# Performance work log

Hardware: AMD Instinct MI355X
Metric: run time of the kernel (lower is better)

Reference implementation:

```python
import jax, jax.numpy as jnp
import numpy as np

B, NUM_HIDDENS, H, W = 32, 128, 64, 64
EMB_DIM = 64
NUM_EMB = 512
COMMITMENT_COST = 0.25


def setup_inputs() -> dict:
    key = jax.random.key(0)
    ks = jax.random.split(key, 5)
    return {
        "bottom_encoding": jax.random.normal(ks[0], (B, NUM_HIDDENS, H, W), jnp.float32),
        "pre_w": jax.random.normal(ks[1], (EMB_DIM, NUM_HIDDENS), jnp.float32) / np.sqrt(NUM_HIDDENS).astype(np.float32),
        "pre_b": jnp.zeros((EMB_DIM,), jnp.float32),
        "codebook": jax.random.uniform(ks[2], (NUM_EMB, EMB_DIM), jnp.float32, -1.0 / NUM_EMB, 1.0 / NUM_EMB),
        "post_w": jax.random.normal(ks[3], (NUM_HIDDENS, EMB_DIM), jnp.float32) / np.sqrt(EMB_DIM).astype(np.float32),
        "post_b": jnp.zeros((NUM_HIDDENS,), jnp.float32),
    }


def reference(bottom_encoding, pre_w, pre_b, codebook, post_w, post_b):
    # pre-VQ 1x1 conv: [B, num_hiddens, H, W] -> [B, emb_dim, H, W]
    x = jnp.einsum('bchw,oc->bohw', bottom_encoding, pre_w) + pre_b[None, :, None, None]
    # BCHW -> BHWC, flatten to [N, D]
    z = jnp.transpose(x, (0, 2, 3, 1))
    flat = z.reshape(-1, EMB_DIM)
    # squared euclidean distances to codebook: [N, K]
    dists = (jnp.sum(flat * flat, axis=1, keepdims=True)
             + jnp.sum(codebook * codebook, axis=1)[None, :]
             - 2.0 * flat @ codebook.T)
    idx = jnp.argmin(dists, axis=1)              # [N] int
    quantized = codebook[idx].reshape(z.shape)   # gather, [B, H, W, D]
    # VQ losses
    e_latent_loss = jnp.mean((jax.lax.stop_gradient(quantized) - z) ** 2)
    q_latent_loss = jnp.mean((quantized - jax.lax.stop_gradient(z)) ** 2)
    loss = q_latent_loss + COMMITMENT_COST * e_latent_loss
    # straight-through estimator
    quantized_st = z + jax.lax.stop_gradient(quantized - z)
    # perplexity of codebook usage
    counts = jnp.zeros((NUM_EMB,), jnp.float32).at[idx].add(1.0)
    avg_probs = counts / idx.shape[0]
    perplexity = jnp.exp(-jnp.sum(avg_probs * jnp.log(avg_probs + 1e-10)))
    # post-VQ 1x1 conv: [B, emb_dim, H, W] -> [B, num_hiddens, H, W]
    qc = jnp.transpose(quantized_st, (0, 3, 1, 2))
    global_decode = jnp.einsum('bchw,oc->bohw', qc, post_w) + post_b[None, :, None, None]
    indices = idx.reshape(B, H, W)
    return loss, global_decode, perplexity, indices
```

## Files before the change

### kernel.cpp

```cpp
#include <hip/hip_runtime.h>

typedef unsigned short u16;
typedef unsigned int u32;
typedef __attribute__((ext_vector_type(8))) short short8v;
typedef __attribute__((ext_vector_type(4))) float f32x4;

#define NPX   131072
#define CHN   128
#define HWN   4096
#define EMB   64
#define NCODE 512

#define WS_HIST 0
#define WS_LOSS 2048
#define WS_CC   4096
#define WS_PWT  8192
#define WS_IDX  40960
#define WS_DT   303104


#define MFMA(a, b, c) __builtin_amdgcn_mfma_f32_16x16x32_bf16((a), (b), (c), 0, 0, 0)

#define SPLIT3(V, HH, MM, LL) {                          \
  u32 zb_ = __float_as_uint(V);                          \
  HH = zb_ >> 16;                                        \
  float fh_ = __uint_as_float(HH << 16);                 \
  float r1_ = __fsub_rn((V), fh_);                       \
  MM = __float_as_uint(r1_) >> 16;                       \
  float fm_ = __uint_as_float(MM << 16);                 \
  float r2_ = __fsub_rn(r1_, fm_);                       \
  LL = __float_as_uint(r2_) >> 16; }

__device__ __forceinline__ float rec3(u32 hb, u32 mb, u32 lb) {
  return __fadd_rn(__fadd_rn(__uint_as_float(hb), __uint_as_float(mb)),
                   __uint_as_float(lb));
}

__global__ __launch_bounds__(256) void vq_init(const float* __restrict__ preW,
                                               const float* __restrict__ cb,
                                               const float* __restrict__ postW,
                                               const float* __restrict__ postB,
                                               float* __restrict__ preWT,
                                               float* __restrict__ cc,
                                               u16* __restrict__ ch,
                                               u16* __restrict__ cm,
                                               u16* __restrict__ cl,
                                               float* __restrict__ DT,
                                               u32* __restrict__ wz) {
  int bid = blockIdx.x, tid = threadIdx.x;
  int idx = bid * 256 + tid;
  {
    int k = idx >> 7, o = idx & 127;
    const float* q = cb + k * EMB;
    const float* w = postW + o * EMB;
    float a0 = 0.f, a1 = 0.f, a2 = 0.f, a3 = 0.f;
#pragma unroll
    for (int dd = 0; dd < 64; dd += 4) {
      a0 = fmaf(q[dd + 0], w[dd + 0], a0);
      a1 = fmaf(q[dd + 1], w[dd + 1], a1);
      a2 = fmaf(q[dd + 2], w[dd + 2], a2);
      a3 = fmaf(q[dd + 3], w[dd + 3], a3);
    }
    DT[(size_t)k * 128 + o] = ((a0 + a1) + (a2 + a3)) + postB[o];
  }
  if (bid == 0) {
    for (int i = tid; i < CHN * EMB; i += 256) {
      int c = i >> 6, d = i & 63;
      preWT[i] = preW[d * CHN + c];
    }
  } else if (bid == 1) {
    for (int t = tid; t < NCODE; t += 256) {
      const float* row = cb + t * EMB;
      float r[8];
#pragma unroll
      for (int j = 0; j < 8; ++j) r[j] = __fmul_rn(row[j], row[j]);
#pragma unroll
      for (int b = 1; b < 8; ++b)
#pragma unroll
        for (int j = 0; j < 8; ++j)
          r[j] = __fadd_rn(r[j], __fmul_rn(row[b * 8 + j], row[b * 8 + j]));
      cc[t] = __fadd_rn(__fadd_rn(__fadd_rn(r[0], r[1]), __fadd_rn(r[2], r[3])),
                        __fadd_rn(__fadd_rn(r[4], r[5]), __fadd_rn(r[6], r[7])));
      int tile = t >> 4, rr = t & 15;
      for (int d = 0; d < EMB; ++d) {
        float v = row[d];
        u32 hh, mm, ll;
        SPLIT3(v, hh, mm, ll)
        size_t ti = (size_t)tile * 1024 + (size_t)(d >> 3) * 128 + rr * 8 + (d & 7);
        ch[ti] = (u16)hh;
        cm[ti] = (u16)mm;
        cl[ti] = (u16)ll;
      }
    }
  } else if (bid == 2) {
    for (int i = tid; i < 513; i += 256) wz[i] = 0;
  }
}

__global__ __launch_bounds__(256) void vq_pre(const float* __restrict__ A,
                                              const float* __restrict__ preWT,
                                              const float* __restrict__ preB,
                                              u16* __restrict__ zh,
                                              u16* __restrict__ zm,
                                              u16* __restrict__ zl) {
  int bid = blockIdx.x;
  int ph = bid & 511, dh = bid >> 9;
  int d0 = dh << 4;
  int p = ph * 256 + threadIdx.x;
  int b = p >> 12, hw = p & 4095;
  const float* Ab = A + (size_t)b * CHN * HWN + hw;

  float z[16];
#pragma unroll
  for (int d = 0; d < 16; ++d) z[d] = 0.f;
  for (int c = 0; c < CHN; c += 4) {
    float a0 = Ab[(size_t)(c + 0) * HWN];
    float a1 = Ab[(size_t)(c + 1) * HWN];
    float a2 = Ab[(size_t)(c + 2) * HWN];
    float a3 = Ab[(size_t)(c + 3) * HWN];
    const float* w = preWT + c * EMB + d0;
#pragma unroll
    for (int d = 0; d < 16; ++d) z[d] = __fadd_rn(z[d], __fmul_rn(a0, w[d]));
    w += EMB;
#pragma unroll
    for (int d = 0; d < 16; ++d) z[d] = __fadd_rn(z[d], __fmul_rn(a1, w[d]));
    w += EMB;
#pragma unroll
    for (int d = 0; d < 16; ++d) z[d] = __fadd_rn(z[d], __fmul_rn(a2, w[d]));
    w += EMB;
#pragma unroll
    for (int d = 0; d < 16; ++d) z[d] = __fadd_rn(z[d], __fmul_rn(a3, w[d]));
  }
#pragma unroll
  for (int d = 0; d < 16; ++d) z[d] = __fadd_rn(z[d], preB[d0 + d]);

  u32 hwd[8], mwd[8], lwd[8];
#pragma unroll
  for (int i = 0; i < 16; ++i) {
    u32 hh, mm, ll;
    SPLIT3(z[i], hh, mm, ll)
    int wdi = i >> 1;
    if ((i & 1) == 0) { hwd[wdi] = hh; mwd[wdi] = mm; lwd[wdi] = ll; }
    else { hwd[wdi] |= hh << 16; mwd[wdi] |= mm << 16; lwd[wdi] |= ll << 16; }
  }
  int tile = p >> 4, rr = p & 15;
  size_t base = (size_t)tile * 1024 + (size_t)(dh * 2) * 128 + rr * 8;
#pragma unroll
  for (int q = 0; q < 2; ++q) {
    size_t off = base + (size_t)q * 128;
    *(uint4*)(zh + off) = make_uint4(hwd[4*q], hwd[4*q+1], hwd[4*q+2], hwd[4*q+3]);
    *(uint4*)(zm + off) = make_uint4(mwd[4*q], mwd[4*q+1], mwd[4*q+2], mwd[4*q+3]);
    *(uint4*)(zl + off) = make_uint4(lwd[4*q], lwd[4*q+1], lwd[4*q+2], lwd[4*q+3]);
  }
}


#define LOADB(T) { size_t ob_ = (size_t)(T) * 1024 + l8;                         \
  Bh0 = *(const short8v*)(ch + ob_); Bh1 = *(const short8v*)(ch + ob_ + 512);    \
  Bm0 = *(const short8v*)(cm + ob_); Bm1 = *(const short8v*)(cm + ob_ + 512);    \
  Bl0 = *(const short8v*)(cl + ob_); Bl1 = *(const short8v*)(cl + ob_ + 512); }

#define COMP(T) {                                                       \
  float ccv_ = scc[((T) << 4) + mcol];                                  \
  _Pragma("unroll")                                                     \
  for (int mt = 0; mt < 2; ++mt) {                                      \
    f32x4 acc = {0.f, 0.f, 0.f, 0.f};                                   \
    acc = MFMA(Ah[mt][0], Bh0, acc); acc = MFMA(Ah[mt][1], Bh1, acc);   \
    acc = MFMA(Am[mt][0], Bh0, acc); acc = MFMA(Am[mt][1], Bh1, acc);   \
    acc = MFMA(Ah[mt][0], Bm0, acc); acc = MFMA(Ah[mt][1], Bm1, acc);   \
    acc = MFMA(Am[mt][0], Bm0, acc); acc = MFMA(Am[mt][1], Bm1, acc);   \
    acc = MFMA(Al[mt][0], Bh0, acc); acc = MFMA(Al[mt][1], Bh1, acc);   \
    acc = MFMA(Ah[mt][0], Bl0, acc); acc = MFMA(Ah[mt][1], Bl1, acc);   \
    acc = MFMA(Al[mt][0], Bm0, acc); acc = MFMA(Al[mt][1], Bm1, acc);   \
    acc = MFMA(Am[mt][0], Bl0, acc); acc = MFMA(Am[mt][1], Bl1, acc);   \
    _Pragma("unroll")                                                   \
    for (int r = 0; r < 4; ++r) {                                       \
      float dist_ = __fadd_rn(__fadd_rn(zzr[mt][r], ccv_), -2.0f * acc[r]); \
      if (dist_ < best[mt][r]) { best[mt][r] = dist_; bidx[mt][r] = ((T) << 4) + mcol; } \
    } } }

__global__ __launch_bounds__(256, 4) void vq_search(const u16* __restrict__ zh,
                                                    const u16* __restrict__ zm,
                                                    const u16* __restrict__ zl,
                                                    const u16* __restrict__ ch,
                                                    const u16* __restrict__ cm,
                                                    const u16* __restrict__ cl,
                                                    const float* __restrict__ cc,
                                                    const float* __restrict__ cb,
                                                    u16* __restrict__ wsIdx,
                                                    float* __restrict__ outIdx,
                                                    float* __restrict__ lossAcc,
                                                    unsigned int* __restrict__ hist) {
  __shared__ float scc[512];
  __shared__ float zs[4][2][16][64];
  __shared__ u16 kb[4][2][16];
  int tid = threadIdx.x;
  scc[tid] = cc[tid];
  scc[tid + 256] = cc[tid + 256];

  int lane = tid & 63, wid = tid >> 6;
  int Mbase = blockIdx.x * 128 + wid * 32;
  int mcol = lane & 15, g = lane >> 4;
  size_t l8 = (size_t)lane * 8;

  short8v Ah[2][2], Am[2][2], Al[2][2];
#pragma unroll
  for (int mt = 0; mt < 2; ++mt) {
    size_t tz = (size_t)((Mbase >> 4) + mt) * 1024 + l8;
    Ah[mt][0] = *(const short8v*)(zh + tz); Ah[mt][1] = *(const short8v*)(zh + tz + 512);
    Am[mt][0] = *(const short8v*)(zm + tz); Am[mt][1] = *(const short8v*)(zm + tz + 512);
    Al[mt][0] = *(const short8v*)(zl + tz); Al[mt][1] = *(const short8v*)(zl + tz + 512);
  }
#pragma unroll
  for (int mt = 0; mt < 2; ++mt)
#pragma unroll
    for (int e = 0; e < 8; ++e) {
      zs[wid][mt][mcol][g * 8 + e] =
          rec3(((u32)(u16)Ah[mt][0][e]) << 16, ((u32)(u16)Am[mt][0][e]) << 16,
               ((u32)(u16)Al[mt][0][e]) << 16);
      zs[wid][mt][mcol][32 + g * 8 + e] =
          rec3(((u32)(u16)Ah[mt][1][e]) << 16, ((u32)(u16)Am[mt][1][e]) << 16,
               ((u32)(u16)Al[mt][1][e]) << 16);
    }
  __syncthreads();

  float zzr[2][4];
#pragma unroll
  for (int mt = 0; mt < 2; ++mt)
#pragma unroll
    for (int r = 0; r < 4; ++r) {
      const float* rowp = &zs[wid][mt][g * 4 + r][0];
      float4 v0 = *(const float4*)(rowp);
      float4 v1 = *(const float4*)(rowp + 4);
      float4 a0, a1;
      a0.x = __fmul_rn(v0.x, v0.x); a0.y = __fmul_rn(v0.y, v0.y);
      a0.z = __fmul_rn(v0.z, v0.z); a0.w = __fmul_rn(v0.w, v0.w);
      a1.x = __fmul_rn(v1.x, v1.x); a1.y = __fmul_rn(v1.y, v1.y);
      a1.z = __fmul_rn(v1.z, v1.z); a1.w = __fmul_rn(v1.w, v1.w);
#pragma unroll
      for (int bb = 1; bb < 8; ++bb) {
        v0 = *(const float4*)(rowp + bb * 8);
        v1 = *(const float4*)(rowp + bb * 8 + 4);
        a0.x = __fadd_rn(a0.x, __fmul_rn(v0.x, v0.x));
        a0.y = __fadd_rn(a0.y, __fmul_rn(v0.y, v0.y));
        a0.z = __fadd_rn(a0.z, __fmul_rn(v0.z, v0.z));
        a0.w = __fadd_rn(a0.w, __fmul_rn(v0.w, v0.w));
        a1.x = __fadd_rn(a1.x, __fmul_rn(v1.x, v1.x));
        a1.y = __fadd_rn(a1.y, __fmul_rn(v1.y, v1.y));
        a1.z = __fadd_rn(a1.z, __fmul_rn(v1.z, v1.z));
        a1.w = __fadd_rn(a1.w, __fmul_rn(v1.w, v1.w));
      }
      zzr[mt][r] = __fadd_rn(
          __fadd_rn(__fadd_rn(a0.x, a0.y), __fadd_rn(a0.z, a0.w)),
          __fadd_rn(__fadd_rn(a1.x, a1.y), __fadd_rn(a1.z, a1.w)));
    }

  float best[2][4];
  int bidx[2][4];
#pragma unroll
  for (int mt = 0; mt < 2; ++mt)
#pragma unroll
    for (int r = 0; r < 4; ++r) { best[mt][r] = 3.4e38f; bidx[mt][r] = 0; }

  short8v Bh0, Bh1, Bm0, Bm1, Bl0, Bl1;
#pragma unroll 2
  for (int t = 0; t < 32; ++t) {
    LOADB(t)
    COMP(t)
  }

#pragma unroll
  for (int mt = 0; mt < 2; ++mt)
#pragma unroll
    for (int r = 0; r < 4; ++r) {
      float v = best[mt][r];
      int ix = bidx[mt][r];
#pragma unroll
      for (int off = 1; off < 16; off <<= 1) {
        float ov = __shfl_xor(v, off, 64);
        int oi = __shfl_xor(ix, off, 64);
        if (ov < v || (ov == v && oi < ix)) { v = ov; ix = oi; }
      }
      if (mcol == 0) {
        int row = Mbase + mt * 16 + g * 4 + r;
        wsIdx[row] = (u16)ix;
        outIdx[row] = (float)ix;
        kb[wid][mt][g * 4 + r] = (u16)ix;
        atomicAdd(&hist[ix], 1u);
      }
    }
  __syncthreads();

  float ls = 0.f;
  if (lane < 32) {
    int mt = lane >> 4, row = lane & 15;
    int krow = kb[wid][mt][row];
    const float4* q4 = (const float4*)(cb + (krow << 6));
    const float* zrow = &zs[wid][mt][row][0];
#pragma unroll
    for (int bb = 0; bb < 8; ++bb) {
      float4 qa = q4[2 * bb], qb = q4[2 * bb + 1];
      float e;
      e = __fsub_rn(qa.x, zrow[8 * bb + 0]); ls = fmaf(e, e, ls);
      e = __fsub_rn(qa.y, zrow[8 * bb + 1]); ls = fmaf(e, e, ls);
      e = __fsub_rn(qa.z, zrow[8 * bb + 2]); ls = fmaf(e, e, ls);
      e = __fsub_rn(qa.w, zrow[8 * bb + 3]); ls = fmaf(e, e, ls);
      e = __fsub_rn(qb.x, zrow[8 * bb + 4]); ls = fmaf(e, e, ls);
      e = __fsub_rn(qb.y, zrow[8 * bb + 5]); ls = fmaf(e, e, ls);
      e = __fsub_rn(qb.z, zrow[8 * bb + 6]); ls = fmaf(e, e, ls);
      e = __fsub_rn(qb.w, zrow[8 * bb + 7]); ls = fmaf(e, e, ls);
    }
  }
#pragma unroll
  for (int off = 32; off; off >>= 1) ls += __shfl_xor(ls, off, 64);
  if (lane == 0) atomicAdd(lossAcc, ls);
}

__global__ __launch_bounds__(256) void vq_decode(const u16* __restrict__ wsIdx,
                                                 const float* __restrict__ DT,
                                                 float* __restrict__ dec) {
  int p = blockIdx.x * 256 + threadIdx.x;
  int b = p >> 12, hw = p & 4095;
  int k = wsIdx[p];
  const float4* Dk = (const float4*)(DT + (size_t)k * 128);
  float* out = dec + (size_t)b * CHN * HWN + hw;
#pragma unroll 4
  for (int oq = 0; oq < 32; ++oq) {
    float4 v = Dk[oq];
    out[(size_t)(4 * oq + 0) * HWN] = v.x;
    out[(size_t)(4 * oq + 1) * HWN] = v.y;
    out[(size_t)(4 * oq + 2) * HWN] = v.z;
    out[(size_t)(4 * oq + 3) * HWN] = v.w;
  }
}

__global__ __launch_bounds__(512) void vq_final(const unsigned int* __restrict__ hist,
                                                const float* __restrict__ lossAcc,
                                                float* __restrict__ outLoss,
                                                float* __restrict__ outPerp) {
  __shared__ float sred[8];
  int t = threadIdx.x;
  float c = (float)hist[t];
  float pavg = c * (1.0f / 131072.0f);
  float term = pavg * logf(pavg + 1e-10f);
#pragma unroll
  for (int off = 32; off; off >>= 1) term += __shfl_xor(term, off, 64);
  if ((t & 63) == 0) sred[t >> 6] = term;
  __syncthreads();
  if (t == 0) {
    float s = 0.f;
    for (int i = 0; i < 8; ++i) s += sred[i];
    *outPerp = expf(-s);
    *outLoss = 1.25f * (*lossAcc) * (1.0f / 8388608.0f);
  }
}

extern "C" void kernel_launch(void* const* d_in, const int* in_sizes, int n_in,
                              void* d_out, int out_size, void* d_ws, size_t ws_size,
                              hipStream_t stream) {
  const float* A     = (const float*)d_in[0];
  const float* preW  = (const float*)d_in[1];
  const float* preB  = (const float*)d_in[2];
  const float* cb    = (const float*)d_in[3];
  const float* postW = (const float*)d_in[4];
  const float* postB = (const float*)d_in[5];
  float* out = (float*)d_out;

  char* ws = (char*)d_ws;
  unsigned int* hist = (unsigned int*)(ws + WS_HIST);
  float* lossAcc = (float*)(ws + WS_LOSS);
  float* cc      = (float*)(ws + WS_CC);
  float* preWT   = (float*)(ws + WS_PWT);
  u16* wsIdx     = (u16*)(ws + WS_IDX);
  float* DT      = (float*)(ws + WS_DT);

  char* outc = (char*)d_out;
  u16* zh = (u16*)(outc + 32);
  u16* zm = (u16*)(outc + 16777248);
  u16* zl = (u16*)(outc + 33554464);
  u16* ch = (u16*)(outc + 50855968);
  u16* cm = (u16*)(outc + 50921504);
  u16* cl = (u16*)(outc + 50987040);

  vq_init<<<256, 256, 0, stream>>>(preW, cb, postW, postB, preWT, cc,
                                   ch, cm, cl, DT, (u32*)ws);
  vq_pre<<<2048, 256, 0, stream>>>(A, preWT, preB, zh, zm, zl);
  vq_search<<<1024, 256, 0, stream>>>(zh, zm, zl, ch, cm, cl, cc, cb,
                                      wsIdx, out + 16777218, lossAcc, hist);
  vq_decode<<<512, 256, 0, stream>>>(wsIdx, DT, out + 1);
  vq_final<<<1, 512, 0, stream>>>(hist, lossAcc, out, out + 16777217);
}
```

Before: 326.7 us.

## Double rows per wave in VQ search, prefetch codebook tiles, split decode channels

The search kernel now handles 64 pixel rows per wave (four M tiles) instead of 32, so each codebook tile loaded from memory is reused across twice as many MFMA row tiles. Codebook loads are double-buffered so the next tile is fetched while the current one is computed. Shared z staging shrinks to padded half-size buffers that are refilled twice. Separately, the decode kernel splits output channels across four blocks per pixel group to get more parallelism. The cost is higher register pressure, with launch bounds lowered to 2 blocks per SM, and extra syncs for the restaging.

```diff
diff --git a/kernel.cpp b/kernel.cpp
--- a/kernel.cpp
+++ b/kernel.cpp
@@ -155,31 +155,52 @@
 }
 
 
-#define LOADB(T) { size_t ob_ = (size_t)(T) * 1024 + l8;                         \
-  Bh0 = *(const short8v*)(ch + ob_); Bh1 = *(const short8v*)(ch + ob_ + 512);    \
-  Bm0 = *(const short8v*)(cm + ob_); Bm1 = *(const short8v*)(cm + ob_ + 512);    \
-  Bl0 = *(const short8v*)(cl + ob_); Bl1 = *(const short8v*)(cl + ob_ + 512); }
-
-#define COMP(T) {                                                       \
+#define LOADB(S, T) {                                                   \
+  size_t ob_ = (size_t)((T) & 31) * 1024 + l8;                          \
+  S##h0 = *(const short8v*)(ch + ob_); S##h1 = *(const short8v*)(ch + ob_ + 512); \
+  S##m0 = *(const short8v*)(cm + ob_); S##m1 = *(const short8v*)(cm + ob_ + 512); \
+  S##l0 = *(const short8v*)(cl + ob_); S##l1 = *(const short8v*)(cl + ob_ + 512); }
+
+#define COMP(S, T) {                                                    \
   float ccv_ = scc[((T) << 4) + mcol];                                  \
   _Pragma("unroll")                                                     \
-  for (int mt = 0; mt < 2; ++mt) {                                      \
+  for (int mt = 0; mt < 4; ++mt) {                                      \
     f32x4 acc = {0.f, 0.f, 0.f, 0.f};                                   \
-    acc = MFMA(Ah[mt][0], Bh0, acc); acc = MFMA(Ah[mt][1], Bh1, acc);   \
-    acc = MFMA(Am[mt][0], Bh0, acc); acc = MFMA(Am[mt][1], Bh1, acc);   \
-    acc = MFMA(Ah[mt][0], Bm0, acc); acc = MFMA(Ah[mt][1], Bm1, acc);   \
-    acc = MFMA(Am[mt][0], Bm0, acc); acc = MFMA(Am[mt][1], Bm1, acc);   \
-    acc = MFMA(Al[mt][0], Bh0, acc); acc = MFMA(Al[mt][1], Bh1, acc);   \
-    acc = MFMA(Ah[mt][0], Bl0, acc); acc = MFMA(Ah[mt][1], Bl1, acc);   \
-    acc = MFMA(Al[mt][0], Bm0, acc); acc = MFMA(Al[mt][1], Bm1, acc);   \
-    acc = MFMA(Am[mt][0], Bl0, acc); acc = MFMA(Am[mt][1], Bl1, acc);   \
+    acc = MFMA(Ah[mt][0], S##h0, acc); acc = MFMA(Ah[mt][1], S##h1, acc); \
+    acc = MFMA(Am[mt][0], S##h0, acc); acc = MFMA(Am[mt][1], S##h1, acc); \
+    acc = MFMA(Ah[mt][0], S##m0, acc); acc = MFMA(Ah[mt][1], S##m1, acc); \
+    acc = MFMA(Am[mt][0], S##m0, acc); acc = MFMA(Am[mt][1], S##m1, acc); \
+    acc = MFMA(Al[mt][0], S##h0, acc); acc = MFMA(Al[mt][1], S##h1, acc); \
+    acc = MFMA(Ah[mt][0], S##l0, acc); acc = MFMA(Ah[mt][1], S##l1, acc); \
+    acc = MFMA(Al[mt][0], S##m0, acc); acc = MFMA(Al[mt][1], S##m1, acc); \
+    acc = MFMA(Am[mt][0], S##l0, acc); acc = MFMA(Am[mt][1], S##l1, acc); \
     _Pragma("unroll")                                                   \
     for (int r = 0; r < 4; ++r) {                                       \
       float dist_ = __fadd_rn(__fadd_rn(zzr[mt][r], ccv_), -2.0f * acc[r]); \
       if (dist_ < best[mt][r]) { best[mt][r] = dist_; bidx[mt][r] = ((T) << 4) + mcol; } \
     } } }
 
-__global__ __launch_bounds__(256, 4) void vq_search(const u16* __restrict__ zh,
+#define STAGE_Z(H) {                                                    \
+  _Pragma("unroll")                                                     \
+  for (int mi = 0; mi < 2; ++mi) {                                      \
+    int mt_ = 2 * (H) + mi;                                             \
+    float* zr_ = &zs[wid][mi * 16 + mcol][0];                           \
+    _Pragma("unroll")                                                   \
+    for (int e = 0; e < 8; e += 2) {                                    \
+      float2 v0_, v1_;                                                  \
+      v0_.x = rec3(((u32)(u16)Ah[mt_][0][e]) << 16, ((u32)(u16)Am[mt_][0][e]) << 16, \
+                   ((u32)(u16)Al[mt_][0][e]) << 16);                    \
+      v0_.y = rec3(((u32)(u16)Ah[mt_][0][e+1]) << 16, ((u32)(u16)Am[mt_][0][e+1]) << 16, \
+                   ((u32)(u16)Al[mt_][0][e+1]) << 16);                  \
+      v1_.x = rec3(((u32)(u16)Ah[mt_][1][e]) << 16, ((u32)(u16)Am[mt_][1][e]) << 16, \
+                   ((u32)(u16)Al[mt_][1][e]) << 16);                    \
+      v1_.y = rec3(((u32)(u16)Ah[mt_][1][e+1]) << 16, ((u32)(u16)Am[mt_][1][e+1]) << 16, \
+                   ((u32)(u16)Al[mt_][1][e+1]) << 16);                  \
+      *(float2*)(zr_ + g * 8 + e) = v0_;                                \
+      *(float2*)(zr_ + 32 + g * 8 + e) = v1_;                           \
+    } } }
+
+__global__ __launch_bounds__(256, 2) void vq_search(const u16* __restrict__ zh,
                                                     const u16* __restrict__ zm,
                                                     const u16* __restrict__ zl,
                                                     const u16* __restrict__ ch,
@@ -192,85 +213,76 @@
                                                     float* __restrict__ lossAcc,
                                                     unsigned int* __restrict__ hist) {
   __shared__ float scc[512];
-  __shared__ float zs[4][2][16][64];
-  __shared__ u16 kb[4][2][16];
+  __shared__ float zs[4][32][66];
   int tid = threadIdx.x;
   scc[tid] = cc[tid];
   scc[tid + 256] = cc[tid + 256];
 
   int lane = tid & 63, wid = tid >> 6;
-  int Mbase = blockIdx.x * 128 + wid * 32;
+  int Mbase = blockIdx.x * 256 + wid * 64;
   int mcol = lane & 15, g = lane >> 4;
   size_t l8 = (size_t)lane * 8;
 
-  short8v Ah[2][2], Am[2][2], Al[2][2];
-#pragma unroll
-  for (int mt = 0; mt < 2; ++mt) {
+  short8v Ah[4][2], Am[4][2], Al[4][2];
+#pragma unroll
+  for (int mt = 0; mt < 4; ++mt) {
     size_t tz = (size_t)((Mbase >> 4) + mt) * 1024 + l8;
     Ah[mt][0] = *(const short8v*)(zh + tz); Ah[mt][1] = *(const short8v*)(zh + tz + 512);
     Am[mt][0] = *(const short8v*)(zm + tz); Am[mt][1] = *(const short8v*)(zm + tz + 512);
     Al[mt][0] = *(const short8v*)(zl + tz); Al[mt][1] = *(const short8v*)(zl + tz + 512);
   }
-#pragma unroll
-  for (int mt = 0; mt < 2; ++mt)
-#pragma unroll
-    for (int e = 0; e < 8; ++e) {
-      zs[wid][mt][mcol][g * 8 + e] =
-          rec3(((u32)(u16)Ah[mt][0][e]) << 16, ((u32)(u16)Am[mt][0][e]) << 16,
-               ((u32)(u16)Al[mt][0][e]) << 16);
-      zs[wid][mt][mcol][32 + g * 8 + e] =
-          rec3(((u32)(u16)Ah[mt][1][e]) << 16, ((u32)(u16)Am[mt][1][e]) << 16,
-               ((u32)(u16)Al[mt][1][e]) << 16);
-    }
   __syncthreads();
 
-  float zzr[2][4];
-#pragma unroll
-  for (int mt = 0; mt < 2; ++mt)
-#pragma unroll
-    for (int r = 0; r < 4; ++r) {
-      const float* rowp = &zs[wid][mt][g * 4 + r][0];
-      float4 v0 = *(const float4*)(rowp);
-      float4 v1 = *(const float4*)(rowp + 4);
-      float4 a0, a1;
-      a0.x = __fmul_rn(v0.x, v0.x); a0.y = __fmul_rn(v0.y, v0.y);
-      a0.z = __fmul_rn(v0.z, v0.z); a0.w = __fmul_rn(v0.w, v0.w);
-      a1.x = __fmul_rn(v1.x, v1.x); a1.y = __fmul_rn(v1.y, v1.y);
-      a1.z = __fmul_rn(v1.z, v1.z); a1.w = __fmul_rn(v1.w, v1.w);
-#pragma unroll
-      for (int bb = 1; bb < 8; ++bb) {
-        v0 = *(const float4*)(rowp + bb * 8);
-        v1 = *(const float4*)(rowp + bb * 8 + 4);
-        a0.x = __fadd_rn(a0.x, __fmul_rn(v0.x, v0.x));
-        a0.y = __fadd_rn(a0.y, __fmul_rn(v0.y, v0.y));
-        a0.z = __fadd_rn(a0.z, __fmul_rn(v0.z, v0.z));
-        a0.w = __fadd_rn(a0.w, __fmul_rn(v0.w, v0.w));
-        a1.x = __fadd_rn(a1.x, __fmul_rn(v1.x, v1.x));
-        a1.y = __fadd_rn(a1.y, __fmul_rn(v1.y, v1.y));
-        a1.z = __fadd_rn(a1.z, __fmul_rn(v1.z, v1.z));
-        a1.w = __fadd_rn(a1.w, __fmul_rn(v1.w, v1.w));
+  float zzr[4][4];
+#pragma unroll
+  for (int h = 0; h < 2; ++h) {
+    STAGE_Z(h)
+    __syncthreads();
+#pragma unroll
+    for (int mi = 0; mi < 2; ++mi) {
+      int mt = 2 * h + mi;
+#pragma unroll
+      for (int r = 0; r < 4; ++r) {
+        const float* rowp = &zs[wid][mi * 16 + g * 4 + r][0];
+        float rr[8];
+#pragma unroll
+        for (int bb = 0; bb < 8; ++bb)
+#pragma unroll
+          for (int j = 0; j < 8; ++j) {
+            float v = rowp[bb * 8 + j];
+            float sq = __fmul_rn(v, v);
+            rr[j] = (bb == 0) ? sq : __fadd_rn(rr[j], sq);
+          }
+        zzr[mt][r] = __fadd_rn(
+            __fadd_rn(__fadd_rn(rr[0], rr[1]), __fadd_rn(rr[2], rr[3])),
+            __fadd_rn(__fadd_rn(rr[4], rr[5]), __fadd_rn(rr[6], rr[7])));
       }
-      zzr[mt][r] = __fadd_rn(
-          __fadd_rn(__fadd_rn(a0.x, a0.y), __fadd_rn(a0.z, a0.w)),
-          __fadd_rn(__fadd_rn(a1.x, a1.y), __fadd_rn(a1.z, a1.w)));
-    }
-
-  float best[2][4];
-  int bidx[2][4];
-#pragma unroll
-  for (int mt = 0; mt < 2; ++mt)
+    }
+    if (h == 0) __syncthreads();
+  }
+
+  float best[4][4];
+  int bidx[4][4];
+#pragma unroll
+  for (int mt = 0; mt < 4; ++mt)
 #pragma unroll
     for (int r = 0; r < 4; ++r) { best[mt][r] = 3.4e38f; bidx[mt][r] = 0; }
 
-  short8v Bh0, Bh1, Bm0, Bm1, Bl0, Bl1;
-#pragma unroll 2
-  for (int t = 0; t < 32; ++t) {
-    LOADB(t)
-    COMP(t)
-  }
-
-#pragma unroll
-  for (int mt = 0; mt < 2; ++mt)
+  short8v PAh0, PAh1, PAm0, PAm1, PAl0, PAl1;
+  short8v PBh0, PBh1, PBm0, PBm1, PBl0, PBl1;
+  LOADB(PA, 0)
+#pragma unroll 1
+  for (int t2 = 0; t2 < 16; ++t2) {
+    int t = t2 * 2;
+    LOADB(PB, t + 1)
+    COMP(PA, t)
+    LOADB(PA, t + 2)
+    COMP(PB, t + 1)
+  }
+
+  int ixr[4][4];
+#pragma unroll
+  for (int mt = 0; mt < 4; ++mt)
 #pragma unroll
     for (int r = 0; r < 4; ++r) {
       float v = best[mt][r];
@@ -281,36 +293,46 @@
         int oi = __shfl_xor(ix, off, 64);
         if (ov < v || (ov == v && oi < ix)) { v = ov; ix = oi; }
       }
+      ixr[mt][r] = ix;
       if (mcol == 0) {
         int row = Mbase + mt * 16 + g * 4 + r;
         wsIdx[row] = (u16)ix;
         outIdx[row] = (float)ix;
-        kb[wid][mt][g * 4 + r] = (u16)ix;
         atomicAdd(&hist[ix], 1u);
       }
     }
-  __syncthreads();
 
   float ls = 0.f;
-  if (lane < 32) {
-    int mt = lane >> 4, row = lane & 15;
-    int krow = kb[wid][mt][row];
-    const float4* q4 = (const float4*)(cb + (krow << 6));
-    const float* zrow = &zs[wid][mt][row][0];
-#pragma unroll
-    for (int bb = 0; bb < 8; ++bb) {
-      float4 qa = q4[2 * bb], qb = q4[2 * bb + 1];
-      float e;
-      e = __fsub_rn(qa.x, zrow[8 * bb + 0]); ls = fmaf(e, e, ls);
-      e = __fsub_rn(qa.y, zrow[8 * bb + 1]); ls = fmaf(e, e, ls);
-      e = __fsub_rn(qa.z, zrow[8 * bb + 2]); ls = fmaf(e, e, ls);
-      e = __fsub_rn(qa.w, zrow[8 * bb + 3]); ls = fmaf(e, e, ls);
-      e = __fsub_rn(qb.x, zrow[8 * bb + 4]); ls = fmaf(e, e, ls);
-      e = __fsub_rn(qb.y, zrow[8 * bb + 5]); ls = fmaf(e, e, ls);
-      e = __fsub_rn(qb.z, zrow[8 * bb + 6]); ls = fmaf(e, e, ls);
-      e = __fsub_rn(qb.w, zrow[8 * bb + 7]); ls = fmaf(e, e, ls);
-    }
-  }
+#pragma unroll
+  for (int hh2 = 1; hh2 >= 0; --hh2) {
+    if (hh2 == 0) { __syncthreads(); STAGE_Z(0) __syncthreads(); }
+#pragma unroll
+    for (int mi = 0; mi < 2; ++mi) {
+      int mt = 2 * hh2 + mi;
+#pragma unroll
+      for (int r = 0; r < 4; ++r) {
+        int krow = ixr[mt][r];
+        const float4* q4 = (const float4*)(cb + (krow << 6));
+        const float* zrow = &zs[wid][mi * 16 + g * 4 + r][0];
+        float rls = 0.f;
+#pragma unroll
+        for (int bb = 0; bb < 8; ++bb) {
+          float4 qa = q4[2 * bb], qb = q4[2 * bb + 1];
+          float e;
+          e = __fsub_rn(qa.x, zrow[8 * bb + 0]); rls = fmaf(e, e, rls);
+          e = __fsub_rn(qa.y, zrow[8 * bb + 1]); rls = fmaf(e, e, rls);
+          e = __fsub_rn(qa.z, zrow[8 * bb + 2]); rls = fmaf(e, e, rls);
+          e = __fsub_rn(qa.w, zrow[8 * bb + 3]); rls = fmaf(e, e, rls);
+          e = __fsub_rn(qb.x, zrow[8 * bb + 4]); rls = fmaf(e, e, rls);
+          e = __fsub_rn(qb.y, zrow[8 * bb + 5]); rls = fmaf(e, e, rls);
+          e = __fsub_rn(qb.z, zrow[8 * bb + 6]); rls = fmaf(e, e, rls);
+          e = __fsub_rn(qb.w, zrow[8 * bb + 7]); rls = fmaf(e, e, rls);
+        }
+        ls += rls;
+      }
+    }
+  }
+  if (mcol != 0) ls = 0.f;
 #pragma unroll
   for (int off = 32; off; off >>= 1) ls += __shfl_xor(ls, off, 64);
   if (lane == 0) atomicAdd(lossAcc, ls);
@@ -319,13 +341,15 @@
 __global__ __launch_bounds__(256) void vq_decode(const u16* __restrict__ wsIdx,
                                                  const float* __restrict__ DT,
                                                  float* __restrict__ dec) {
-  int p = blockIdx.x * 256 + threadIdx.x;
+  int bid = blockIdx.x;
+  int och = bid & 3, ph = bid >> 2;
+  int p = ph * 256 + threadIdx.x;
   int b = p >> 12, hw = p & 4095;
   int k = wsIdx[p];
   const float4* Dk = (const float4*)(DT + (size_t)k * 128);
   float* out = dec + (size_t)b * CHN * HWN + hw;
-#pragma unroll 4
-  for (int oq = 0; oq < 32; ++oq) {
+#pragma unroll
+  for (int oq = och * 8; oq < och * 8 + 8; ++oq) {
     float4 v = Dk[oq];
     out[(size_t)(4 * oq + 0) * HWN] = v.x;
     out[(size_t)(4 * oq + 1) * HWN] = v.y;
@@ -385,8 +409,8 @@
   vq_init<<<256, 256, 0, stream>>>(preW, cb, postW, postB, preWT, cc,
                                    ch, cm, cl, DT, (u32*)ws);
   vq_pre<<<2048, 256, 0, stream>>>(A, preWT, preB, zh, zm, zl);
-  vq_search<<<1024, 256, 0, stream>>>(zh, zm, zl, ch, cm, cl, cc, cb,
-                                      wsIdx, out + 16777218, lossAcc, hist);
-  vq_decode<<<512, 256, 0, stream>>>(wsIdx, DT, out + 1);
+  vq_search<<<512, 256, 0, stream>>>(zh, zm, zl, ch, cm, cl, cc, cb,
+                                     wsIdx, out + 16777218, lossAcc, hist);
+  vq_decode<<<2048, 256, 0, stream>>>(wsIdx, DT, out + 1);
   vq_final<<<1, 512, 0, stream>>>(hist, lossAcc, out, out + 16777217);
 }
```

Result: slower. 340.8 us (+4.3%).
